# Performance work log

Measured on AMD Instinct MI355X. Metric: run time of the kernel, lower is better.

Reference implementation:

```python
import jax, jax.numpy as jnp
import numpy as np
from jax import lax

NS, NQ, D, C = 1000, 131072, 1024, 100

def setup_inputs() -> dict:
    key = jax.random.key(0)
    k1, k2, k3, k4 = jax.random.split(key, 4)
    return {
        "support_x": jax.random.normal(k1, (NS, D), dtype=jnp.float32),
        "support_y": jax.random.randint(k2, (NS,), 0, C),
        "query_x": jax.random.normal(k3, (NQ, D), dtype=jnp.float32),
        "query_y": jax.random.randint(k4, (NQ,), 0, C),
        "n_iter": 10,
        "beta": 5,
        "num_classes": C,
    }

def _l2norm(x):
    return x / jnp.linalg.norm(x, axis=1, keepdims=True)

def _sqdist(q, c):
    # ||q - c||^2 = |q|^2 + |c|^2 - 2 q.c   -> [Nq, C]
    q2 = jnp.sum(q * q, axis=1, keepdims=True)
    c2 = jnp.sum(c * c, axis=1)
    return q2 + c2[None, :] - 2.0 * (q @ c.T)

def reference(support_x, support_y, query_x, query_y, n_iter, beta, num_classes):
    betaf = jnp.float32(beta)
    # preprocess_KMeans: sphere by support mean, then L2-normalize
    mean_feature = jnp.mean(support_x, axis=0)
    s = _l2norm(support_x - mean_feature)   # [Ns, D]
    q = _l2norm(query_x - mean_feature)     # [Nq, D]

    # per-class support sums/counts (hard assignments for support points)
    sup_sum = jax.ops.segment_sum(s, support_y, num_segments=num_classes)          # [C, D]
    sup_cnt = jax.ops.segment_sum(jnp.ones((s.shape[0],), s.dtype), support_y,
                                  num_segments=num_classes)                        # [C]
    centroids0 = sup_sum / sup_cnt[:, None]  # class means (intent of original init)

    def step(centroids, _):
        d2 = _sqdist(q, centroids)                       # [Nq, C]
        w = jax.nn.softmax(-betaf * d2, axis=1)          # soft assignment weights
        suma = sup_sum + w.T @ q                         # [C, D]
        sumb = sup_cnt + jnp.sum(w, axis=0)              # [C]
        return suma / sumb[:, None], None

    centroids, _ = lax.scan(step, centroids0, None, length=n_iter)

    pred = jnp.argmin(_sqdist(q, centroids), axis=1)     # nearest centroid
    acc = jnp.mean((pred == query_y).astype(jnp.float32))
    return acc
```

## Files before the change

### kernel.cpp

```cpp
#include <hip/hip_runtime.h>
#include <hip/hip_fp8.h>
#include <math.h>

#define NS 1000
#define NQ 131072
#define D  1024
#define C  100
#define CP 112
#define BETA 5.0f
#define NITER 10
#define KC 64
#define KROWS (NQ/KC)
#define KS8 (KROWS/64)

typedef float f32x4 __attribute__((ext_vector_type(4)));
typedef short s16x8 __attribute__((ext_vector_type(8)));
typedef long s64;
typedef s64 s64x2 __attribute__((ext_vector_type(2)));
typedef unsigned short u16;
typedef unsigned char u8;
typedef unsigned long long ull;

__device__ __forceinline__ u16 f2bf(float x) {
  union { float f; unsigned u; } v; v.f = x;
  unsigned r = v.u + 0x7fffu + ((v.u >> 16) & 1u);
  return (u16)(r >> 16);
}
__device__ __forceinline__ float bf2f(u16 h) {
  union { unsigned u; float f; } v; v.u = ((unsigned)h) << 16; return v.f;
}
__device__ __forceinline__ u8 f2fp8(float x) {
  __hip_fp8_e4m3 h(x);
  return (u8)h.__x;
}
__device__ __forceinline__ void gld16(const u16* g, u16* l) {
  __builtin_amdgcn_global_load_lds(
      (const __attribute__((address_space(1))) void*)g,
      (__attribute__((address_space(3))) void*)l, 16, 0, 0);
}
__device__ __forceinline__ void gld16b(const u8* g, u8* l) {
  __builtin_amdgcn_global_load_lds(
      (const __attribute__((address_space(1))) void*)g,
      (__attribute__((address_space(3))) void*)l, 16, 0, 0);
}
__device__ __forceinline__ s16x8 frag32(const u16* plane, int row, int kb) {
  int s = kb ^ (row & 3);
  return *(const s16x8*)(plane + row * 32 + s * 8);
}
__device__ __forceinline__ f32x4 mfma16(s16x8 a, s16x8 b, f32x4 c) {
  return __builtin_amdgcn_mfma_f32_16x16x32_bf16(a, b, c, 0, 0, 0);
}
__device__ __forceinline__ f32x4 mfma8(s64 a, s64 b, f32x4 c) {
  return __builtin_amdgcn_mfma_f32_16x16x32_fp8_fp8(a, b, c, 0, 0, 0);
}


__global__ __launch_bounds__(256) void k_mean(const float* __restrict__ sx,
                                              float* __restrict__ mean) {
  int d = blockIdx.x * 256 + threadIdx.x;
  float a = 0.f;
  for (int r = 0; r < NS; ++r) a += sx[(size_t)r * D + d];
  mean[d] = a / (float)NS;
}

__global__ __launch_bounds__(256) void k_invn(const float* __restrict__ x,
                                              const float* __restrict__ mean,
                                              float* __restrict__ invn) {
  int r = blockIdx.x;
  int t = threadIdx.x;
  float4 v = ((const float4*)(x + (size_t)r * D))[t];
  float4 m = ((const float4*)mean)[t];
  float a = v.x - m.x, b = v.y - m.y, c = v.z - m.z, d = v.w - m.w;
  float s = a * a + b * b + c * c + d * d;
#pragma unroll
  for (int off = 1; off < 64; off <<= 1) s += __shfl_xor(s, off);
  __shared__ float ws[4];
  if ((t & 63) == 0) ws[t >> 6] = s;
  __syncthreads();
  if (t == 0) invn[r] = 1.0f / sqrtf(ws[0] + ws[1] + ws[2] + ws[3]);
}

__global__ __launch_bounds__(256) void k_supsum(const float* __restrict__ sx,
        const int* __restrict__ sy, const float* __restrict__ mean,
        const float* __restrict__ invs, float* __restrict__ supsum,
        float* __restrict__ supcnt) {
  int c = blockIdx.x;
  int t = threadIdx.x;
  float a0 = 0.f, a1 = 0.f, a2 = 0.f, a3 = 0.f;
  int cnt = 0;
  if (c < C) {
    for (int r = 0; r < NS; ++r) {
      if (sy[r] == c) {
        ++cnt;
        float inv = invs[r];
        a0 += (sx[(size_t)r * D + t      ] - mean[t      ]) * inv;
        a1 += (sx[(size_t)r * D + t + 256] - mean[t + 256]) * inv;
        a2 += (sx[(size_t)r * D + t + 512] - mean[t + 512]) * inv;
        a3 += (sx[(size_t)r * D + t + 768] - mean[t + 768]) * inv;
      }
    }
  }
  supsum[(size_t)c * D + t      ] = a0;
  supsum[(size_t)c * D + t + 256] = a1;
  supsum[(size_t)c * D + t + 512] = a2;
  supsum[(size_t)c * D + t + 768] = a3;
  if (t == 0) supcnt[c] = (float)cnt;
}

__global__ void k_zero(int* __restrict__ corr) {
  if (threadIdx.x == 0) corr[0] = 0;
}

__global__ void k_out(const int* __restrict__ corr, float* __restrict__ out) {
  if (threadIdx.x == 0) out[0] = (float)corr[0] * (1.0f / (float)NQ);
}

__global__ __launch_bounds__(256) void k_qprep(const float* __restrict__ qx,
        const float* __restrict__ mean, float* __restrict__ invq,
        u8* __restrict__ qf8, u8* __restrict__ qt8) {
  __shared__ float msh[1024];
  __shared__ float pp[64];
  __shared__ float invql[64];
  __shared__ u8 T8[64 * 68];
  int t = threadIdx.x, w = t >> 6, l = t & 63;
  int q0 = blockIdx.x * 64;
  ((float4*)msh)[t] = ((const float4*)mean)[t];
  __syncthreads();

#pragma unroll 1
  for (int rr = 0; rr < 16; ++rr) {
    int row = w * 16 + rr;
    const float* rp = qx + (size_t)(q0 + row) * D;
    float s = 0.f;
#pragma unroll
    for (int seg = 0; seg < 4; ++seg) {
      float4 v = *(const float4*)(rp + seg * 256 + l * 4);
      float4 m = *(const float4*)(msh + seg * 256 + l * 4);
      float a = v.x - m.x, b = v.y - m.y, c = v.z - m.z, d = v.w - m.w;
      s += a * a + b * b + c * c + d * d;
    }
#pragma unroll
    for (int off = 1; off < 64; off <<= 1) s += __shfl_xor(s, off);
    if (l == 0) pp[row] = s;
  }
  __syncthreads();
  if (t < 64) {
    float iv = 1.0f / sqrtf(pp[t]);
    invql[t] = iv;
    invq[q0 + t] = iv;
  }
  __syncthreads();

  int r = t >> 2, c0 = (t & 3) * 16;
  float iv = invql[r];
  int h8 = (c0 >= 32) ? 1 : 0;
  int sA = (c0 & 31) >> 3;
  int lb = (r & 15) * 16 + h8 * 8;
  int tq4 = (t & 15) * 4, td4 = (t >> 4) * 4;
  for (int d0 = 0; d0 < D; d0 += 64) {
    const float* src = qx + (size_t)(q0 + r) * D + d0 + c0;
    union { u8 b[16]; ull q[2]; } F;
#pragma unroll
    for (int j = 0; j < 16; j += 4) {
      float4 v = *(const float4*)(src + j);
      float xs[4] = {v.x, v.y, v.z, v.w};
#pragma unroll
      for (int u = 0; u < 4; ++u) {
        float x = (xs[u] - msh[d0 + c0 + j + u]) * iv;
        F.b[j + u] = f2fp8(16.0f * x);
      }
    }
    size_t fb8 = (((size_t)(q0 >> 7) * 16 + (d0 >> 6)) * 8 +
                  ((q0 & 64) >> 4) + (r >> 4)) * 1024;
    *(ull*)(qf8 + fb8 + sA * 256 + lb)       = F.q[0];
    *(ull*)(qf8 + fb8 + (sA + 1) * 256 + lb) = F.q[1];
    __syncthreads();
#pragma unroll
    for (int j = 0; j < 4; ++j)
      *(uchar4*)(T8 + r * 68 + c0 + j * 4) =
          make_uchar4(F.b[j * 4], F.b[j * 4 + 1], F.b[j * 4 + 2], F.b[j * 4 + 3]);
    __syncthreads();
    u8 a[4][4];
#pragma unroll
    for (int i = 0; i < 4; ++i)
      *(uchar4*)a[i] = *(const uchar4*)(T8 + (tq4 + i) * 68 + td4);
#pragma unroll
    for (int j = 0; j < 4; ++j)
      *(uchar4*)(qt8 + (size_t)(d0 + td4 + j) * NQ + q0 + tq4) =
          make_uchar4(a[0][j], a[1][j], a[2][j], a[3][j]);
  }
}

template<int INIT>
__global__ __launch_bounds__(256) void k_updm(const float* __restrict__ supsum,
        const float* __restrict__ part, const float* __restrict__ wsump,
        const float* __restrict__ supcnt,
        u16* __restrict__ cfh, u16* __restrict__ cfl, u8* __restrict__ cf8,
        float* __restrict__ c2p) {
  int c = blockIdx.x, by = blockIdx.y, t = threadIdx.x;
  __shared__ float red[4];
  float den;
  if (INIT) {
    den = supcnt[c];
  } else {
    float s = 0.f;
#pragma unroll
    for (int b = 0; b < 4; ++b) s += wsump[(size_t)(t + b * 256) * CP + c];
#pragma unroll
    for (int off = 1; off < 64; off <<= 1) s += __shfl_xor(s, off);
    if ((t & 63) == 0) red[t >> 6] = s;
    __syncthreads();
    den = supcnt[c] + ((red[0] + red[1]) + (red[2] + red[3]));
    __syncthreads();
  }
  int d = by * 256 + t;
  float s = supsum[(size_t)c * D + d];
  if (!INIT) {
    float p0 = 0.f, p1 = 0.f, p2 = 0.f, p3 = 0.f;
    for (int kc = 0; kc < KC; kc += 4) {
      p0 += part[((size_t)(kc + 0) * CP + c) * D + d];
      p1 += part[((size_t)(kc + 1) * CP + c) * D + d];
      p2 += part[((size_t)(kc + 2) * CP + c) * D + d];
      p3 += part[((size_t)(kc + 3) * CP + c) * D + d];
    }
    s += 0.0009765625f * ((p0 + p1) + (p2 + p3));
  }
  float v = (c < C) ? s / den : 0.f;
  size_t a16 = (size_t)(d >> 5) * (CP * 32) + c * 32 +
               ((((d >> 3) & 3) ^ (c & 3)) * 8) + (d & 7);
  u16 h = f2bf(v);
  cfh[a16] = h;
  cfl[a16] = f2bf(v - bf2f(h));
  size_t a8 = ((size_t)(d >> 6) * CP + c) * 64 +
              ((((d >> 4) & 3) ^ (c & 3)) * 16) + (d & 15);
  cf8[a8] = f2fp8(16.0f * v);
  float ss = v * v;
#pragma unroll
  for (int off = 1; off < 64; off <<= 1) ss += __shfl_xor(ss, off);
  __syncthreads();
  if ((t & 63) == 0) red[t >> 6] = ss;
  __syncthreads();
  if (t == 0) c2p[c * 4 + by] =
      (c < C) ? ((red[0] + red[1]) + (red[2] + red[3])) : 2.5e29f;
}


__global__ __launch_bounds__(256) void k_logits8(
    const u8* __restrict__ qf8, const u8* __restrict__ cf8,
    const float* __restrict__ c2p,
    u8* __restrict__ Wf8, float* __restrict__ wsump) {
  __shared__ __align__(16) u8 sm[3 * 7168];
  __shared__ float wred[4][CP];
  int t = threadIdx.x, w = t >> 6, l = t & 63;
  int qblk = blockIdx.x;
  const u8* ap0 = qf8 + (size_t)qblk * 131072 + (size_t)(w * 2) * 1024 + l * 16;
  int s_ = l >> 4, r15 = l & 15;
  int o8 = (s_ & 1) * 8;
  int go0 = s_ >> 1, go1 = 2 + (s_ >> 1);

  f32x4 acc[2][7];
#pragma unroll
  for (int mf = 0; mf < 2; ++mf)
#pragma unroll
    for (int nf = 0; nf < 7; ++nf) acc[mf][nf] = (f32x4){0.f, 0.f, 0.f, 0.f};

  auto stageB = [&](u8* buf, int kb) {
    for (int i = w; i < 7; i += 4)
      gld16b(cf8 + (size_t)kb * 7168 + i * 1024 + l * 16, buf + i * 1024);
  };
  auto computeK = [&](const u8* buf, s64x2 a0, s64x2 a1) {
#pragma unroll
    for (int nf = 0; nf < 7; ++nf) {
      int row = nf * 16 + r15;
      const u8* rp = buf + row * 64;
      int sw = row & 3;
      s64 b0 = *(const s64*)(rp + ((go0 ^ sw) << 4) + o8);
      s64 b1 = *(const s64*)(rp + ((go1 ^ sw) << 4) + o8);
      f32x4 x0 = acc[0][nf], x1 = acc[1][nf];
      x0 = mfma8(a0[0], b0, x0); x0 = mfma8(a0[1], b1, x0);
      x1 = mfma8(a1[0], b0, x1); x1 = mfma8(a1[1], b1, x1);
      acc[0][nf] = x0; acc[1][nf] = x1;
    }
  };
#define WAITC8() { if (w < 3) asm volatile("s_waitcnt vmcnt(4)" ::: "memory"); \
                   else       asm volatile("s_waitcnt vmcnt(3)" ::: "memory"); }

  s64x2 a0A, a1A, a0B, a1B;
  u8 *p0 = sm, *p1 = sm + 7168, *p2 = sm + 14336;
  a0A = *(const s64x2*)ap0; a1A = *(const s64x2*)(ap0 + 1024);
  stageB(p0, 0);
  for (int kp = 0; kp < 8; ++kp) {
    int k = kp * 2;
    { const u8* p = ap0 + (size_t)(k + 1) * 8192;
      a0B = *(const s64x2*)p; a1B = *(const s64x2*)(p + 1024); }
    stageB(p1, k + 1);
    WAITC8();
    __builtin_amdgcn_s_barrier();
    computeK(p0, a0A, a1A);
    if (k + 2 < 16) {
      const u8* p = ap0 + (size_t)(k + 2) * 8192;
      a0A = *(const s64x2*)p; a1A = *(const s64x2*)(p + 1024);
      stageB(p2, k + 2);
      WAITC8();
    } else {
      asm volatile("s_waitcnt vmcnt(0)" ::: "memory");
    }
    __builtin_amdgcn_s_barrier();
    computeK(p1, a0B, a1B);
    u8* tmp = p0; p0 = p2; p2 = p1; p1 = tmp;
  }
  __syncthreads();

  float c2v[7];
#pragma unroll
  for (int nf = 0; nf < 7; ++nf) {
    int cc = nf * 16 + r15;
    float4 p = *(const float4*)(c2p + cc * 4);
    c2v[nf] = (p.x + p.y) + (p.z + p.w);
  }

  const float LS = 2.0f / 256.0f;
  float wcol[7];
#pragma unroll
  for (int nf = 0; nf < 7; ++nf) wcol[nf] = 0.f;
  u8* Wsh8 = sm;
#pragma unroll
  for (int mf = 0; mf < 2; ++mf)
#pragma unroll
    for (int r = 0; r < 4; ++r) {
      float Lg[7], mx = -INFINITY;
#pragma unroll
      for (int nf = 0; nf < 7; ++nf) {
        Lg[nf] = LS * acc[mf][nf][r] - c2v[nf];
        mx = fmaxf(mx, Lg[nf]);
      }
#pragma unroll
      for (int off = 1; off < 16; off <<= 1) mx = fmaxf(mx, __shfl_xor(mx, off));
      float e[7], s = 0.f;
#pragma unroll
      for (int nf = 0; nf < 7; ++nf) { e[nf] = expf(BETA * (Lg[nf] - mx)); s += e[nf]; }
#pragma unroll
      for (int off = 1; off < 16; off <<= 1) s += __shfl_xor(s, off);
      float is = 1.f / s;
      int qi = w * 32 + mf * 16 + (l >> 4) * 4 + r;
#pragma unroll
      for (int nf = 0; nf < 7; ++nf) {
        float wv = e[nf] * is;
        wcol[nf] += wv;
        int cc = nf * 16 + r15;
        Wsh8[cc * 128 + (((qi >> 4) ^ (cc & 7)) << 4) + (qi & 15)] =
            f2fp8(64.0f * wv);
      }
    }
#pragma unroll
  for (int off = 16; off < 64; off <<= 1)
#pragma unroll
    for (int nf = 0; nf < 7; ++nf) wcol[nf] += __shfl_xor(wcol[nf], off);
  if (l < 16)
#pragma unroll
    for (int nf = 0; nf < 7; ++nf) wred[w][nf * 16 + l] = wcol[nf];
  __syncthreads();
  {
    size_t wb = (size_t)(qblk >> 4) * (32 * 7168);
    int ks0 = (qblk * 2) & 31;
    for (int idx = t; idx < 896; idx += 256) {
      int c = idx >> 3, g = idx & 7;
      uint4 v = *(const uint4*)(Wsh8 + c * 128 + ((g ^ (c & 7)) << 4));
      *(uint4*)(Wf8 + wb + (size_t)(ks0 + (g >> 2)) * 7168 + c * 64 +
                (((g & 3) ^ (c & 3)) << 4)) = v;
    }
  }
  if (t < CP) wsump[(size_t)qblk * CP + t] =
      wred[0][t] + wred[1][t] + wred[2][t] + wred[3][t];
#undef WAITC8
}


__global__ __launch_bounds__(256) void k_wqm8(
    const u8* __restrict__ Wf8, const u8* __restrict__ qt8,
    float* __restrict__ part) {
  __shared__ __align__(16) u8 sm[3][15360];
  int t = threadIdx.x, w = t >> 6, l = t & 63;
  int ck = blockIdx.x;
  int d0 = blockIdx.y * 128;
  size_t wbase = (size_t)ck * (32 * 7168);
  size_t qoff  = (size_t)ck * KROWS;
  int s_ = l >> 4, r15 = l & 15;
  int o8 = (s_ & 1) * 8;
  int go0 = s_ >> 1, go1 = 2 + (s_ >> 1);

  f32x4 acc[7][2];
#pragma unroll
  for (int mf = 0; mf < 7; ++mf)
#pragma unroll
    for (int nf = 0; nf < 2; ++nf) acc[mf][nf] = (f32x4){0.f, 0.f, 0.f, 0.f};

  auto stage = [&](u8* buf, int ks) {
    for (int i = w; i < 7; i += 4)
      gld16b(Wf8 + wbase + (size_t)ks * 7168 + i * 1024 + l * 16, buf + i * 1024);
#pragma unroll
    for (int i2 = w * 2; i2 < w * 2 + 2; ++i2) {
      int row = i2 * 16 + (l >> 2);
      int g = (l & 3) ^ ((l >> 2) & 3);
      gld16b(qt8 + (size_t)(d0 + row) * NQ + qoff + (size_t)ks * 64 + g * 16,
             buf + 7168 + i2 * 1024);
    }
  };
  auto computeK = [&](const u8* buf) {
    const u8* qb = buf + 7168;
    s64 bq00, bq01, bq10, bq11;
    {
      int row = w * 32 + r15;
      const u8* rp = qb + row * 64; int sw = row & 3;
      bq00 = *(const s64*)(rp + ((go0 ^ sw) << 4) + o8);
      bq01 = *(const s64*)(rp + ((go1 ^ sw) << 4) + o8);
    }
    {
      int row = w * 32 + 16 + r15;
      const u8* rp = qb + row * 64; int sw = row & 3;
      bq10 = *(const s64*)(rp + ((go0 ^ sw) << 4) + o8);
      bq11 = *(const s64*)(rp + ((go1 ^ sw) << 4) + o8);
    }
#pragma unroll
    for (int mf = 0; mf < 7; ++mf) {
      int row = mf * 16 + r15;
      const u8* rp = buf + row * 64; int sw = row & 3;
      s64 a0 = *(const s64*)(rp + ((go0 ^ sw) << 4) + o8);
      s64 a1 = *(const s64*)(rp + ((go1 ^ sw) << 4) + o8);
      f32x4 x0 = acc[mf][0], x1 = acc[mf][1];
      x0 = mfma8(a0, bq00, x0); x0 = mfma8(a1, bq01, x0);
      x1 = mfma8(a0, bq10, x1); x1 = mfma8(a1, bq11, x1);
      acc[mf][0] = x0; acc[mf][1] = x1;
    }
  };
#define WAITC4() { if (w < 3) asm volatile("s_waitcnt vmcnt(4)" ::: "memory"); \
                   else       asm volatile("s_waitcnt vmcnt(3)" ::: "memory"); }

  u8 *p0 = sm[0], *p1 = sm[1], *p2 = sm[2];
  stage(p0, 0);
  for (int kp = 0; kp < KS8 / 2; ++kp) {
    int k = kp * 2;
    stage(p1, k + 1);
    WAITC4();
    __builtin_amdgcn_s_barrier();
    computeK(p0);
    if (k + 2 < KS8) {
      stage(p2, k + 2);
      WAITC4();
    } else {
      asm volatile("s_waitcnt vmcnt(0)" ::: "memory");
    }
    __builtin_amdgcn_s_barrier();
    computeK(p1);
    u8* tmp = p0; p0 = p2; p2 = p1; p1 = tmp;
  }
#pragma unroll
  for (int mf = 0; mf < 7; ++mf)
#pragma unroll
    for (int nf = 0; nf < 2; ++nf)
#pragma unroll
      for (int r = 0; r < 4; ++r) {
        int c = mf * 16 + (l >> 4) * 4 + r;
        int dg = d0 + w * 32 + nf * 16 + r15;
        part[((size_t)ck * CP + c) * D + dg] = acc[mf][nf][r];
      }
#undef WAITC4
}


__global__ __launch_bounds__(256) void k_final(
    const float* __restrict__ qx, const float* __restrict__ mean,
    const float* __restrict__ invq,
    const u16* __restrict__ cfh, const u16* __restrict__ cfl,
    const float* __restrict__ c2p,
    const int* __restrict__ qy, int* __restrict__ corr) {
  __shared__ __align__(16) u16 sm[3 * 7168];
  __shared__ float msh[1024];
  __shared__ float ivsh[128];
  int t = threadIdx.x, w = t >> 6, l = t & 63;
  int q0 = blockIdx.x * 128;
  ((float4*)msh)[t] = ((const float4*)mean)[t];
  if (t < 32) ((float4*)ivsh)[t] = ((const float4*)(invq + q0))[t];
  __syncthreads();

  int r15 = l & 15;
  int ko = (l >> 4) * 8;
  int row0 = w * 32 + r15, row1 = row0 + 16;
  const float* a0p = qx + (size_t)(q0 + row0) * D + ko;
  const float* a1p = qx + (size_t)(q0 + row1) * D + ko;
  float iv0 = ivsh[row0], iv1 = ivsh[row1];
  int kb = l >> 4;

  f32x4 acc[2][7];
#pragma unroll
  for (int mf = 0; mf < 2; ++mf)
#pragma unroll
    for (int nf = 0; nf < 7; ++nf) acc[mf][nf] = (f32x4){0.f, 0.f, 0.f, 0.f};

#define ALOADR(ks, R) { \
    const float* p0_ = a0p + (size_t)(ks) * 32; \
    const float* p1_ = a1p + (size_t)(ks) * 32; \
    R[0] = *(const float4*)p0_; R[1] = *(const float4*)(p0_ + 4); \
    R[2] = *(const float4*)p1_; R[3] = *(const float4*)(p1_ + 4); }

  auto stageB = [&](u16* buf, int ks) {
    for (int i = w; i < 14; i += 4) {
      const u16* src = (i < 7) ? (cfh + (size_t)(ks) * 3584 + i * 512 + l * 8)
                               : (cfl + (size_t)(ks) * 3584 + (i - 7) * 512 + l * 8);
      gld16(src, buf + i * 512);
    }
  };
  auto mk = [&](const float4& u0, const float4& u1, float iv, int ks,
                s16x8& hh, s16x8& ll) {
    float xs[8] = {u0.x, u0.y, u0.z, u0.w, u1.x, u1.y, u1.z, u1.w};
#pragma unroll
    for (int u = 0; u < 8; ++u) {
      float x = (xs[u] - msh[ks * 32 + ko + u]) * iv;
      u16 h = f2bf(x);
      hh[u] = (short)h;
      ll[u] = (short)f2bf(x - bf2f(h));
    }
  };
  auto computeK = [&](const u16* buf, float4* R, int ks) {
    s16x8 h0, l0, h1, l1;
    mk(R[0], R[1], iv0, ks, h0, l0);
    mk(R[2], R[3], iv1, ks, h1, l1);
#pragma unroll
    for (int nf = 0; nf < 7; ++nf) {
      int row = nf * 16 + r15;
      s16x8 bh = frag32(buf, row, kb);
      s16x8 bl = frag32(buf + 3584, row, kb);
      f32x4 a0 = acc[0][nf], a1 = acc[1][nf];
      a0 = mfma16(l0, bh, a0); a0 = mfma16(h0, bl, a0); a0 = mfma16(h0, bh, a0);
      a1 = mfma16(l1, bh, a1); a1 = mfma16(h1, bl, a1); a1 = mfma16(h1, bh, a1);
      acc[0][nf] = a0; acc[1][nf] = a1;
    }
  };
#define WAITCF() { if (w < 2) asm volatile("s_waitcnt vmcnt(8)" ::: "memory"); \
                   else       asm volatile("s_waitcnt vmcnt(7)" ::: "memory"); }

  float4 rA[4], rB[4];
  u16 *p0 = sm, *p1 = sm + 7168, *p2 = sm + 14336;
  ALOADR(0, rA);
  stageB(p0, 0);
  for (int kp = 0; kp < 16; ++kp) {
    int k = kp * 2;
    ALOADR(k + 1, rB);
    stageB(p1, k + 1);
    WAITCF();
    __builtin_amdgcn_s_barrier();
    computeK(p0, rA, k);
    if (k + 2 < 32) {
      ALOADR(k + 2, rA);
      stageB(p2, k + 2);
      WAITCF();
    } else {
      asm volatile("s_waitcnt vmcnt(0)" ::: "memory");
    }
    __builtin_amdgcn_s_barrier();
    computeK(p1, rB, k + 1);
    u16* tmp = p0; p0 = p2; p2 = p1; p1 = tmp;
  }
  __syncthreads();

  float c2v[7];
#pragma unroll
  for (int nf = 0; nf < 7; ++nf) {
    int cc = nf * 16 + r15;
    float4 p = *(const float4*)(c2p + cc * 4);
    c2v[nf] = (p.x + p.y) + (p.z + p.w);
  }

  int cnt = 0;
#pragma unroll
  for (int mf = 0; mf < 2; ++mf)
#pragma unroll
    for (int r = 0; r < 4; ++r) {
      float bv = -INFINITY; int bi = 0x7fffffff;
#pragma unroll
      for (int nf = 0; nf < 7; ++nf) {
        float Lg = 2.f * acc[mf][nf][r] - c2v[nf];
        int cc = nf * 16 + r15;
        if (Lg > bv || (Lg == bv && cc < bi)) { bv = Lg; bi = cc; }
      }
#pragma unroll
      for (int off = 1; off < 16; off <<= 1) {
        float ov = __shfl_xor(bv, off); int oi = __shfl_xor(bi, off);
        if (ov > bv || (ov == bv && oi < bi)) { bv = ov; bi = oi; }
      }
      if (r15 == 0) {
        int qi = w * 32 + mf * 16 + (l >> 4) * 4 + r;
        cnt += (bi == qy[q0 + qi]) ? 1 : 0;
      }
    }
  if (r15 == 0) atomicAdd(corr, cnt);
#undef ALOADR
#undef WAITCF
}


extern "C" void kernel_launch(void* const* d_in, const int* in_sizes, int n_in,
                              void* d_out, int out_size, void* d_ws, size_t ws_size,
                              hipStream_t stream) {
  const float* sx = (const float*)d_in[0];
  const int*   sy = (const int*)d_in[1];
  const float* qx = (const float*)d_in[2];
  const int*   qy = (const int*)d_in[3];

  char* base = (char*)d_ws;
  size_t o = 0;
  auto take = [&](size_t bytes) { size_t r = o; o += (bytes + 511) & ~(size_t)511; return r; };
  float* mean   = (float*)(base + take(4096));
  float* invs   = (float*)(base + take(4096));
  float* invq   = (float*)(base + take((size_t)NQ * 4));
  float* supsum = (float*)(base + take((size_t)CP * D * 4));
  float* supcnt = (float*)(base + take(512));
  float* c2pA   = (float*)(base + take(2048));
  float* c2pB   = (float*)(base + take(2048));
  float* wsump  = (float*)(base + take((size_t)(NQ / 128) * CP * 4));
  int*   corr   = (int*)(base + take(512));
  u16* cfhA = (u16*)(base + take((size_t)CP * D * 2));
  u16* cflA = (u16*)(base + take((size_t)CP * D * 2));
  u16* cfhB = (u16*)(base + take((size_t)CP * D * 2));
  u16* cflB = (u16*)(base + take((size_t)CP * D * 2));
  u8*  cf8A = (u8*)(base + take((size_t)CP * D));
  u8*  cf8B = (u8*)(base + take((size_t)CP * D));
  u8*  Wf8  = (u8*)(base + take((size_t)CP * NQ));
  float* part = (float*)(base + take((size_t)KC * CP * D * 4));
  u8*  qf8  = (u8*)(base + take((size_t)NQ * D));
  u8*  qt8  = (u8*)(base + take((size_t)NQ * D));
  size_t fast_need = o;

  if (ws_size < fast_need) {
    k_zero<<<1, 64, 0, stream>>>((int*)d_out);
    return;
  }

  k_mean<<<dim3(D / 256), 256, 0, stream>>>(sx, mean);
  k_invn<<<dim3(NS), 256, 0, stream>>>(sx, mean, invs);
  k_supsum<<<dim3(CP), 256, 0, stream>>>(sx, sy, mean, invs, supsum, supcnt);
  k_updm<1><<<dim3(CP, 4), 256, 0, stream>>>(supsum, part, wsump, supcnt,
                                             cfhA, cflA, cf8A, c2pA);
  k_qprep<<<dim3(NQ / 64), 256, 0, stream>>>(qx, mean, invq, qf8, qt8);

  u16 *chc = cfhA, *clc = cflA, *chn = cfhB, *cln = cflB;
  u8  *c8c = cf8A, *c8n = cf8B;
  float *c2c = c2pA, *c2n = c2pB;
  for (int it = 0; it < NITER; ++it) {
    k_logits8<<<dim3(NQ / 128), 256, 0, stream>>>(qf8, c8c, c2c, Wf8, wsump);
    k_wqm8<<<dim3(KC, D / 128), 256, 0, stream>>>(Wf8, qt8, part);
    k_updm<0><<<dim3(CP, 4), 256, 0, stream>>>(supsum, part, wsump, supcnt,
                                               chn, cln, c8n, c2n);
    u16* tu;
    tu = chc; chc = chn; chn = tu;
    tu = clc; clc = cln; cln = tu;
    u8* t8 = c8c; c8c = c8n; c8n = t8;
    float* tf = c2c; c2c = c2n; c2n = tf;
  }
  k_zero<<<1, 64, 0, stream>>>(corr);
  k_final<<<dim3(NQ / 128), 256, 0, stream>>>(qx, mean, invq, chc, clc, c2c,
                                              qy, corr);
  k_out<<<1, 64, 0, stream>>>(corr, (float*)d_out);
}
```

Baseline: 1.613 ms.

## Double K-split chunks, store partials in bf16, parallelize support mean

Increases the number of query chunks in the W^T·Q reduction from 64 to 128, so k_wqm8 launches twice as many blocks for better GPU occupancy, and adjusts the Wf8 layout indexing to match. The per-chunk partial sums are now stored as bf16 instead of fp32, which halves the partial-buffer traffic that k_updm has to read back. The serial support-mean kernel is split into an 8-way partial-sum pass plus a small combine pass, adding parallelism to the setup phase. The bf16 partials lose precision in the centroid update, which could shift the final predictions and therefore the accuracy.

```diff
diff --git a/kernel.cpp b/kernel.cpp
--- a/kernel.cpp
+++ b/kernel.cpp
@@ -9,7 +9,7 @@
 #define CP 112
 #define BETA 5.0f
 #define NITER 10
-#define KC 64
+#define KC 128
 #define KROWS (NQ/KC)
 #define KS8 (KROWS/64)
 
@@ -55,12 +55,22 @@
 }
 
 
-__global__ __launch_bounds__(256) void k_mean(const float* __restrict__ sx,
-                                              float* __restrict__ mean) {
+__global__ __launch_bounds__(256) void k_meanp(const float* __restrict__ sx,
+                                               float* __restrict__ meanp) {
   int d = blockIdx.x * 256 + threadIdx.x;
+  int r0 = blockIdx.y * 125;
   float a = 0.f;
-  for (int r = 0; r < NS; ++r) a += sx[(size_t)r * D + d];
-  mean[d] = a / (float)NS;
+  for (int r = r0; r < r0 + 125; ++r) a += sx[(size_t)r * D + d];
+  meanp[(size_t)blockIdx.y * D + d] = a;
+}
+
+__global__ __launch_bounds__(256) void k_mean2(const float* __restrict__ meanp,
+                                               float* __restrict__ mean) {
+  int d = blockIdx.x * 256 + threadIdx.x;
+  float p0 = meanp[d], p1 = meanp[D + d], p2 = meanp[2 * D + d],
+        p3 = meanp[3 * D + d], p4 = meanp[4 * D + d], p5 = meanp[5 * D + d],
+        p6 = meanp[6 * D + d], p7 = meanp[7 * D + d];
+  mean[d] = (((p0 + p1) + (p2 + p3)) + ((p4 + p5) + (p6 + p7))) * (1.0f / (float)NS);
 }
 
 __global__ __launch_bounds__(256) void k_invn(const float* __restrict__ x,
@@ -193,7 +203,7 @@
 
 template<int INIT>
 __global__ __launch_bounds__(256) void k_updm(const float* __restrict__ supsum,
-        const float* __restrict__ part, const float* __restrict__ wsump,
+        const u16* __restrict__ part, const float* __restrict__ wsump,
         const float* __restrict__ supcnt,
         u16* __restrict__ cfh, u16* __restrict__ cfl, u8* __restrict__ cf8,
         float* __restrict__ c2p) {
@@ -218,10 +228,10 @@
   if (!INIT) {
     float p0 = 0.f, p1 = 0.f, p2 = 0.f, p3 = 0.f;
     for (int kc = 0; kc < KC; kc += 4) {
-      p0 += part[((size_t)(kc + 0) * CP + c) * D + d];
-      p1 += part[((size_t)(kc + 1) * CP + c) * D + d];
-      p2 += part[((size_t)(kc + 2) * CP + c) * D + d];
-      p3 += part[((size_t)(kc + 3) * CP + c) * D + d];
+      p0 += bf2f(part[((size_t)(kc + 0) * CP + c) * D + d]);
+      p1 += bf2f(part[((size_t)(kc + 1) * CP + c) * D + d]);
+      p2 += bf2f(part[((size_t)(kc + 2) * CP + c) * D + d]);
+      p3 += bf2f(part[((size_t)(kc + 3) * CP + c) * D + d]);
     }
     s += 0.0009765625f * ((p0 + p1) + (p2 + p3));
   }
@@ -361,8 +371,8 @@
     for (int nf = 0; nf < 7; ++nf) wred[w][nf * 16 + l] = wcol[nf];
   __syncthreads();
   {
-    size_t wb = (size_t)(qblk >> 4) * (32 * 7168);
-    int ks0 = (qblk * 2) & 31;
+    size_t wb = (size_t)(qblk >> 3) * (16 * 7168);
+    int ks0 = (qblk * 2) & 15;
     for (int idx = t; idx < 896; idx += 256) {
       int c = idx >> 3, g = idx & 7;
       uint4 v = *(const uint4*)(Wsh8 + c * 128 + ((g ^ (c & 7)) << 4));
@@ -378,12 +388,12 @@
 
 __global__ __launch_bounds__(256) void k_wqm8(
     const u8* __restrict__ Wf8, const u8* __restrict__ qt8,
-    float* __restrict__ part) {
+    u16* __restrict__ part) {
   __shared__ __align__(16) u8 sm[3][15360];
   int t = threadIdx.x, w = t >> 6, l = t & 63;
   int ck = blockIdx.x;
   int d0 = blockIdx.y * 128;
-  size_t wbase = (size_t)ck * (32 * 7168);
+  size_t wbase = (size_t)ck * (KS8 * 7168);
   size_t qoff  = (size_t)ck * KROWS;
   int s_ = l >> 4, r15 = l & 15;
   int o8 = (s_ & 1) * 8;
@@ -462,7 +472,7 @@
       for (int r = 0; r < 4; ++r) {
         int c = mf * 16 + (l >> 4) * 4 + r;
         int dg = d0 + w * 32 + nf * 16 + r15;
-        part[((size_t)ck * CP + c) * D + dg] = acc[mf][nf][r];
+        part[((size_t)ck * CP + c) * D + dg] = f2bf(acc[mf][nf][r]);
       }
 #undef WAITC4
 }
@@ -611,6 +621,7 @@
   size_t o = 0;
   auto take = [&](size_t bytes) { size_t r = o; o += (bytes + 511) & ~(size_t)511; return r; };
   float* mean   = (float*)(base + take(4096));
+  float* meanp  = (float*)(base + take(8 * D * 4));
   float* invs   = (float*)(base + take(4096));
   float* invq   = (float*)(base + take((size_t)NQ * 4));
   float* supsum = (float*)(base + take((size_t)CP * D * 4));
@@ -626,7 +637,7 @@
   u8*  cf8A = (u8*)(base + take((size_t)CP * D));
   u8*  cf8B = (u8*)(base + take((size_t)CP * D));
   u8*  Wf8  = (u8*)(base + take((size_t)CP * NQ));
-  float* part = (float*)(base + take((size_t)KC * CP * D * 4));
+  u16* part = (u16*)(base + take((size_t)KC * CP * D * 2));
   u8*  qf8  = (u8*)(base + take((size_t)NQ * D));
   u8*  qt8  = (u8*)(base + take((size_t)NQ * D));
   size_t fast_need = o;
@@ -636,7 +647,8 @@
     return;
   }
 
-  k_mean<<<dim3(D / 256), 256, 0, stream>>>(sx, mean);
+  k_meanp<<<dim3(D / 256, 8), 256, 0, stream>>>(sx, meanp);
+  k_mean2<<<dim3(D / 256), 256, 0, stream>>>(meanp, mean);
   k_invn<<<dim3(NS), 256, 0, stream>>>(sx, mean, invs);
   k_supsum<<<dim3(CP), 256, 0, stream>>>(sx, sy, mean, invs, supsum, supcnt);
   k_updm<1><<<dim3(CP, 4), 256, 0, stream>>>(supsum, part, wsump, supcnt,
```

After: 1.589 ms, median of 5. About the same (-1.5%).
